# Optimization experiments

Measured on AMD Instinct MI355X. Metric: run time of the kernel, lower is better.

## Reference

```python
import jax, jax.numpy as jnp
import numpy as np

N_NODES = 100000
N_EDGES = 1600000
N_FEAT = 128
HIDDEN = 64
N_CLASSES = 16


def setup_inputs() -> dict:
    key = jax.random.key(0)
    ks = jax.random.split(key, 8)
    x = jax.random.normal(ks[0], (N_NODES, N_FEAT), dtype=jnp.float32)
    edge_index = jax.random.randint(ks[1], (2, N_EDGES), 0, N_NODES, dtype=jnp.int64)
    def glorot(k, shape):
        lim = float(np.sqrt(6.0 / (shape[0] + shape[1])))
        return jax.random.uniform(k, shape, jnp.float32, -lim, lim)
    return {
        "x": x,
        "edge_index": edge_index,
        "W0": glorot(ks[2], (N_FEAT, HIDDEN)), "b0": jnp.zeros((HIDDEN,), jnp.float32),
        "W1": glorot(ks[3], (HIDDEN, HIDDEN)), "b1": jnp.zeros((HIDDEN,), jnp.float32),
        "W2": glorot(ks[4], (HIDDEN, 2)),      "b2": jnp.zeros((2,), jnp.float32),
        "Wc": glorot(ks[5], (2, N_CLASSES)),   "bc": jnp.zeros((N_CLASSES,), jnp.float32),
    }


def _gcn_conv(x, W, b, src, dst, norm, n_nodes):
    # GCNConv: D^{-1/2} (A + I) D^{-1/2} X W + b, edges already include self-loops
    h = x @ W                                  # transform first (small dim)
    msg = h[src] * norm[:, None]               # gather + per-edge scale
    agg = jax.ops.segment_sum(msg, dst, num_segments=n_nodes)  # scatter-add
    return agg + b


def reference(x, edge_index, W0, b0, W1, b1, W2, b2, Wc, bc):
    n = x.shape[0]
    loops = jnp.arange(n, dtype=edge_index.dtype)
    src = jnp.concatenate([edge_index[0], loops])
    dst = jnp.concatenate([edge_index[1], loops])
    # degree on destination (col), including self-loops
    deg = jax.ops.segment_sum(jnp.ones_like(dst, dtype=x.dtype), dst, num_segments=n)
    dis = jnp.where(deg > 0, jax.lax.rsqrt(deg), 0.0)
    norm = dis[src] * dis[dst]

    h = _gcn_conv(x, W0, b0, src, dst, norm, n)              # layer 0, no activation
    h = jnp.tanh(_gcn_conv(h, W1, b1, src, dst, norm, n))    # layer 1
    h = jnp.tanh(_gcn_conv(h, W2, b2, src, dst, norm, n))    # layer 2 -> [N, 2]
    embeddings = h
    out = embeddings @ Wc + bc                               # [N, num_classes]
    return (out, embeddings)
```

## Files before the change

kernel.cpp:

```cpp
#include <hip/hip_runtime.h>


#define NF 128
#define NH 64
#define NPB 256
#define MAXNB 512
#define CAP 6144
#define A1G 1024

__global__ void k_init0(const int* __restrict__ ei, int* __restrict__ fmt,
                        int* __restrict__ ccnt, int nb16) {
    int i = blockIdx.x * 256 + threadIdx.x;
    if (i < nb16) ccnt[i] = 0;
    if (i == 0) {
        int f = 1;
        #pragma unroll
        for (int k = 1; k < 32; k += 2) if (ei[k] != 0) f = 0;
        *fmt = f;
    }
}

__global__ void __launch_bounds__(256) k_coarse(
        const int* __restrict__ ei, const int* __restrict__ fmt,
        int* __restrict__ ccnt, int* __restrict__ blockbase, int E, int NB) {
    __shared__ int h[MAXNB];
    int sh = *fmt;
    for (int i = threadIdx.x; i < NB; i += 256) h[i] = 0;
    __syncthreads();
    for (long long e = (long long)blockIdx.x * 256 + threadIdx.x; e < E;
         e += (long long)A1G * 256) {
        int d = ei[(long long)(E + e) << sh];
        atomicAdd(&h[d >> 8], 1);
    }
    __syncthreads();
    for (int b = threadIdx.x; b < NB; b += 256) {
        int c = h[b];
        int base = (c > 0) ? atomicAdd(&ccnt[b * 16], c) : 0;
        blockbase[(long long)blockIdx.x * NB + b] = base;
    }
}

__global__ void __launch_bounds__(512) k_cscan(
        const int* __restrict__ ccnt, int* __restrict__ cstart, int NB) {
    __shared__ int s[512];
    int t = threadIdx.x;
    int c = (t < NB) ? ccnt[t * 16] : 0;
    s[t] = c;
    __syncthreads();
    for (int off = 1; off < 512; off <<= 1) {
        int v = s[t];
        int u = (t >= off) ? s[t - off] : 0;
        __syncthreads();
        s[t] = v + u;
        __syncthreads();
    }
    if (t < NB) cstart[t] = s[t] - c;
}

__global__ void __launch_bounds__(256) k_cscatter(
        const int* __restrict__ ei, const int* __restrict__ fmt,
        const int* __restrict__ cstart, const int* __restrict__ blockbase,
        int* __restrict__ pairs, int E, int NB) {
    __shared__ int h[MAXNB];
    __shared__ int bb[MAXNB];
    int sh = *fmt;
    for (int i = threadIdx.x; i < NB; i += 256) {
        h[i] = 0;
        bb[i] = cstart[i] + blockbase[(long long)blockIdx.x * NB + i];
    }
    __syncthreads();
    for (long long e = (long long)blockIdx.x * 256 + threadIdx.x; e < E;
         e += (long long)A1G * 256) {
        int s = ei[(long long)e << sh];
        int d = ei[(long long)(E + e) << sh];
        int b = d >> 8;
        int r = atomicAdd(&h[b], 1);
        pairs[bb[b] + r] = s | ((d & 255) << 17);
    }
}

__global__ void __launch_bounds__(256) k_bucket(
        const int* __restrict__ pairs, const int* __restrict__ ccnt,
        const int* __restrict__ cstart, int* __restrict__ esrc,
        int* __restrict__ cnt, int* __restrict__ start, float* __restrict__ dis,
        int N) {
    __shared__ int words[CAP];
    __shared__ unsigned char rk[CAP];
    __shared__ int h[NPB];
    __shared__ int hs[NPB];
    int b = blockIdx.x;
    int cs = cstart[b];
    int ec = ccnt[b * 16];
    if (ec > CAP) ec = CAP;
    int t = threadIdx.x;
    for (int i = t; i < ec; i += 256) words[i] = pairs[cs + i];
    h[t] = 0;
    __syncthreads();
    for (int i = t; i < ec; i += 256) {
        int ld = words[i] >> 17;
        rk[i] = (unsigned char)atomicAdd(&h[ld], 1);
    }
    __syncthreads();
    int c = h[t];
    hs[t] = c;
    __syncthreads();
    for (int off = 1; off < 256; off <<= 1) {
        int v = hs[t];
        int u = (t >= off) ? hs[t - off] : 0;
        __syncthreads();
        hs[t] = v + u;
        __syncthreads();
    }
    int node = b * NPB + t;
    if (node < N) {
        cnt[node] = c;
        start[node] = cs + hs[t] - c;
        dis[node] = rsqrtf(1.0f + (float)c);
    }
    for (int i = t; i < ec; i += 256) {
        int w = words[i];
        int ld = w >> 17;
        esrc[cs + (hs[ld] - h[ld]) + rk[i]] = w & 0x1FFFF;
    }
}

#define KP3 68
__global__ void __launch_bounds__(256) k_gemm128(
        const float* __restrict__ X, const float* __restrict__ W,
        const float* __restrict__ dis, short* __restrict__ T16,
        float* __restrict__ rs, int n) {
    __shared__ float xs[64 * KP3];
    __shared__ float Ws[64 * NH];
    __shared__ int rmax[64];
    if (threadIdx.x < 64) rmax[threadIdx.x] = 0;
    long long rowbase = (long long)blockIdx.x * 64;
    int c0 = (threadIdx.x & 15) * 4;
    int r0 = (threadIdx.x >> 4) * 4;
    float4 a0{0,0,0,0}, a1{0,0,0,0}, a2{0,0,0,0}, a3{0,0,0,0};
    #pragma unroll
    for (int ph = 0; ph < 2; ++ph) {
        if (ph) __syncthreads();
        const float4* Wp4 = (const float4*)(W + (long long)ph * 64 * NH);
        for (int i = threadIdx.x; i < 64 * NH / 4; i += 256)
            ((float4*)Ws)[i] = Wp4[i];
        const float* Xp = X + rowbase * NF + ph * 64;
        for (int i = threadIdx.x; i < 1024; i += 256) {
            int r = i >> 4, kk = (i & 15) << 2;
            float4 v = (rowbase + r < n)
                           ? *(const float4*)(Xp + r * NF + kk)
                           : make_float4(0.f, 0.f, 0.f, 0.f);
            *(float4*)&xs[r * KP3 + kk] = v;
        }
        __syncthreads();
        const float* x0 = &xs[(r0 + 0) * KP3];
        const float* x1 = &xs[(r0 + 1) * KP3];
        const float* x2 = &xs[(r0 + 2) * KP3];
        const float* x3 = &xs[(r0 + 3) * KP3];
        const float* Wp0 = &Ws[c0];
        #pragma unroll 4
        for (int k4 = 0; k4 < 16; ++k4) {
            float4 xv0 = *(const float4*)(x0 + k4 * 4);
            float4 xv1 = *(const float4*)(x1 + k4 * 4);
            float4 xv2 = *(const float4*)(x2 + k4 * 4);
            float4 xv3 = *(const float4*)(x3 + k4 * 4);
            float4 wa = *(const float4*)(Wp0 + (k4 * 4 + 0) * NH);
            float4 wb = *(const float4*)(Wp0 + (k4 * 4 + 1) * NH);
            float4 wc = *(const float4*)(Wp0 + (k4 * 4 + 2) * NH);
            float4 wd = *(const float4*)(Wp0 + (k4 * 4 + 3) * NH);
            a0.x += xv0.x * wa.x; a0.y += xv0.x * wa.y; a0.z += xv0.x * wa.z; a0.w += xv0.x * wa.w;
            a1.x += xv1.x * wa.x; a1.y += xv1.x * wa.y; a1.z += xv1.x * wa.z; a1.w += xv1.x * wa.w;
            a2.x += xv2.x * wa.x; a2.y += xv2.x * wa.y; a2.z += xv2.x * wa.z; a2.w += xv2.x * wa.w;
            a3.x += xv3.x * wa.x; a3.y += xv3.x * wa.y; a3.z += xv3.x * wa.z; a3.w += xv3.x * wa.w;
            a0.x += xv0.y * wb.x; a0.y += xv0.y * wb.y; a0.z += xv0.y * wb.z; a0.w += xv0.y * wb.w;
            a1.x += xv1.y * wb.x; a1.y += xv1.y * wb.y; a1.z += xv1.y * wb.z; a1.w += xv1.y * wb.w;
            a2.x += xv2.y * wb.x; a2.y += xv2.y * wb.y; a2.z += xv2.y * wb.z; a2.w += xv2.y * wb.w;
            a3.x += xv3.y * wb.x; a3.y += xv3.y * wb.y; a3.z += xv3.y * wb.z; a3.w += xv3.y * wb.w;
            a0.x += xv0.z * wc.x; a0.y += xv0.z * wc.y; a0.z += xv0.z * wc.z; a0.w += xv0.z * wc.w;
            a1.x += xv1.z * wc.x; a1.y += xv1.z * wc.y; a1.z += xv1.z * wc.z; a1.w += xv1.z * wc.w;
            a2.x += xv2.z * wc.x; a2.y += xv2.z * wc.y; a2.z += xv2.z * wc.z; a2.w += xv2.z * wc.w;
            a3.x += xv3.z * wc.x; a3.y += xv3.z * wc.y; a3.z += xv3.z * wc.z; a3.w += xv3.z * wc.w;
            a0.x += xv0.w * wd.x; a0.y += xv0.w * wd.y; a0.z += xv0.w * wd.z; a0.w += xv0.w * wd.w;
            a1.x += xv1.w * wd.x; a1.y += xv1.w * wd.y; a1.z += xv1.w * wd.z; a1.w += xv1.w * wd.w;
            a2.x += xv2.w * wd.x; a2.y += xv2.w * wd.y; a2.z += xv2.w * wd.z; a2.w += xv2.w * wd.w;
            a3.x += xv3.w * wd.x; a3.y += xv3.w * wd.y; a3.z += xv3.w * wd.z; a3.w += xv3.w * wd.w;
        }
    }
    int row = (int)rowbase + r0;
    float d0 = (row + 0 < n) ? dis[row + 0] : 0.0f;
    float d1 = (row + 1 < n) ? dis[row + 1] : 0.0f;
    float d2 = (row + 2 < n) ? dis[row + 2] : 0.0f;
    float d3 = (row + 3 < n) ? dis[row + 3] : 0.0f;
    a0.x *= d0; a0.y *= d0; a0.z *= d0; a0.w *= d0;
    a1.x *= d1; a1.y *= d1; a1.z *= d1; a1.w *= d1;
    a2.x *= d2; a2.y *= d2; a2.z *= d2; a2.w *= d2;
    a3.x *= d3; a3.y *= d3; a3.z *= d3; a3.w *= d3;
    float m0 = fmaxf(fmaxf(fabsf(a0.x), fabsf(a0.y)), fmaxf(fabsf(a0.z), fabsf(a0.w)));
    float m1 = fmaxf(fmaxf(fabsf(a1.x), fabsf(a1.y)), fmaxf(fabsf(a1.z), fabsf(a1.w)));
    float m2 = fmaxf(fmaxf(fabsf(a2.x), fabsf(a2.y)), fmaxf(fabsf(a2.z), fabsf(a2.w)));
    float m3 = fmaxf(fmaxf(fabsf(a3.x), fabsf(a3.y)), fmaxf(fabsf(a3.z), fabsf(a3.w)));
    atomicMax(&rmax[r0 + 0], __float_as_int(m0));
    atomicMax(&rmax[r0 + 1], __float_as_int(m1));
    atomicMax(&rmax[r0 + 2], __float_as_int(m2));
    atomicMax(&rmax[r0 + 3], __float_as_int(m3));
    __syncthreads();
    float M0 = __int_as_float(rmax[r0 + 0]);
    float M1 = __int_as_float(rmax[r0 + 1]);
    float M2 = __int_as_float(rmax[r0 + 2]);
    float M3 = __int_as_float(rmax[r0 + 3]);
    float i0 = 32767.0f / fmaxf(M0, 1e-20f);
    float i1 = 32767.0f / fmaxf(M1, 1e-20f);
    float i2 = 32767.0f / fmaxf(M2, 1e-20f);
    float i3 = 32767.0f / fmaxf(M3, 1e-20f);
    const float ks = 1.0f / 32767.0f;
    if (row + 0 < n) {
        short4 q = { (short)__float2int_rn(a0.x * i0), (short)__float2int_rn(a0.y * i0),
                     (short)__float2int_rn(a0.z * i0), (short)__float2int_rn(a0.w * i0) };
        *(short4*)&T16[(long long)(row + 0) * NH + c0] = q;
        if (c0 == 0) rs[row + 0] = M0 * ks;
    }
    if (row + 1 < n) {
        short4 q = { (short)__float2int_rn(a1.x * i1), (short)__float2int_rn(a1.y * i1),
                     (short)__float2int_rn(a1.z * i1), (short)__float2int_rn(a1.w * i1) };
        *(short4*)&T16[(long long)(row + 1) * NH + c0] = q;
        if (c0 == 0) rs[row + 1] = M1 * ks;
    }
    if (row + 2 < n) {
        short4 q = { (short)__float2int_rn(a2.x * i2), (short)__float2int_rn(a2.y * i2),
                     (short)__float2int_rn(a2.z * i2), (short)__float2int_rn(a2.w * i2) };
        *(short4*)&T16[(long long)(row + 2) * NH + c0] = q;
        if (c0 == 0) rs[row + 2] = M2 * ks;
    }
    if (row + 3 < n) {
        short4 q = { (short)__float2int_rn(a3.x * i3), (short)__float2int_rn(a3.y * i3),
                     (short)__float2int_rn(a3.z * i3), (short)__float2int_rn(a3.w * i3) };
        *(short4*)&T16[(long long)(row + 3) * NH + c0] = q;
        if (c0 == 0) rs[row + 3] = M3 * ks;
    }
}

#define EDGE_A(J) {                                                           \
    int s_ = __builtin_amdgcn_readlane(sA, (J));                              \
    float f_ = __int_as_float(__builtin_amdgcn_readlane(fAb, (J)));           \
    accA = fmaf(f_, (float)(T + s_ * NH)[lane], accA); }
#define EDGE_B(J) {                                                           \
    int s_ = __builtin_amdgcn_readlane(sB, (J));                              \
    float f_ = __int_as_float(__builtin_amdgcn_readlane(fBb, (J)));           \
    accB = fmaf(f_, (float)(T + s_ * NH)[lane], accB); }

#define SEG_GATHER2                                                           \
    int lane = threadIdx.x & 63;                                              \
    int na = blockIdx.x * 8 + (threadIdx.x >> 6) * 2;                         \
    int nb_ = na + 1;                                                         \
    if (na >= n) return;                                                      \
    bool hasB = (nb_ < n);                                                    \
    float dia = dis[na];                                                      \
    float dib = hasB ? dis[nb_] : 0.0f;                                       \
    int ga = cnt[na], sta = start[na];                                        \
    int gb = hasB ? cnt[nb_] : 0;                                             \
    int stb = hasB ? start[nb_] : 0;                                          \
    float accA = rs[na] * (float)T[na * NH + lane];                           \
    float accB = hasB ? rs[nb_] * (float)T[nb_ * NH + lane] : 0.0f;           \
    int gmax = ga > gb ? ga : gb;                                             \
    for (int base = 0; base < gmax; base += 64) {                             \
        int ma = ga - base; ma = ma < 0 ? 0 : (ma > 64 ? 64 : ma);            \
        int mb = gb - base; mb = mb < 0 ? 0 : (mb > 64 ? 64 : mb);            \
        int sA = 0, sB = 0; float fA = 0.0f, fB = 0.0f;                       \
        if (lane < ma) { sA = esrc[sta + base + lane]; fA = rs[sA]; }         \
        if (lane < mb) { sB = esrc[stb + base + lane]; fB = rs[sB]; }         \
        int fAb = __float_as_int(fA), fBb = __float_as_int(fB);               \
        int mmin = ma < mb ? ma : mb;                                         \
        int j = 0;                                                            \
        for (; j + 3 < mmin; j += 4) {                                        \
            EDGE_A(j + 0) EDGE_B(j + 0)                                       \
            EDGE_A(j + 1) EDGE_B(j + 1)                                       \
            EDGE_A(j + 2) EDGE_B(j + 2)                                       \
            EDGE_A(j + 3) EDGE_B(j + 3)                                       \
        }                                                                     \
        int jA = j, jB = j;                                                   \
        for (; jA + 3 < ma; jA += 4) {                                        \
            EDGE_A(jA + 0) EDGE_A(jA + 1) EDGE_A(jA + 2) EDGE_A(jA + 3)       \
        }                                                                     \
        for (; jA < ma; ++jA) EDGE_A(jA)                                      \
        for (; jB + 3 < mb; jB += 4) {                                        \
            EDGE_B(jB + 0) EDGE_B(jB + 1) EDGE_B(jB + 2) EDGE_B(jB + 3)       \
        }                                                                     \
        for (; jB < mb; ++jB) EDGE_B(jB)                                      \
    }

__global__ void __launch_bounds__(256) k_seg0t(
        const short* __restrict__ T, const float* __restrict__ rs,
        const int* __restrict__ esrc, const int* __restrict__ start,
        const int* __restrict__ cnt, const float* __restrict__ dis,
        const float* __restrict__ b0, const float* __restrict__ W1,
        short* __restrict__ To, float* __restrict__ rso, int n) {
    __shared__ float W1s[NH * NH];
    for (int i = threadIdx.x; i < NH * NH / 4; i += 256)
        ((float4*)W1s)[i] = ((const float4*)W1)[i];
    __syncthreads();
    SEG_GATHER2
    float bv = b0[lane];
    float hA = dia * accA + bv;
    float hB = dib * accB + bv;
    float oA = 0.0f, oB = 0.0f;
    #pragma unroll
    for (int c = 0; c < 64; ++c) {
        float wv = W1s[c * NH + lane];
        float ha = __int_as_float(__builtin_amdgcn_readlane(__float_as_int(hA), c));
        float hb = __int_as_float(__builtin_amdgcn_readlane(__float_as_int(hB), c));
        oA = fmaf(ha, wv, oA);
        oB = fmaf(hb, wv, oB);
    }
    oA *= dia;
    oB *= dib;
    float mA = fabsf(oA), mB = fabsf(oB);
    #pragma unroll
    for (int msk = 32; msk; msk >>= 1) {
        mA = fmaxf(mA, __shfl_xor(mA, msk, 64));
        mB = fmaxf(mB, __shfl_xor(mB, msk, 64));
    }
    float iA = 32767.0f / fmaxf(mA, 1e-20f);
    float iB = 32767.0f / fmaxf(mB, 1e-20f);
    const float ks = 1.0f / 32767.0f;
    To[(long long)na * NH + lane] = (short)__float2int_rn(oA * iA);
    if (lane == 0) rso[na] = mA * ks;
    if (hasB) {
        To[(long long)nb_ * NH + lane] = (short)__float2int_rn(oB * iB);
        if (lane == 0) rso[nb_] = mB * ks;
    }
}

__global__ void __launch_bounds__(256) k_seg1f(
        const short* __restrict__ T, const float* __restrict__ rs,
        const int* __restrict__ esrc, const int* __restrict__ start,
        const int* __restrict__ cnt, const float* __restrict__ dis,
        const float* __restrict__ b1, const float* __restrict__ W2,
        float2* __restrict__ t2, int n) {
    SEG_GATHER2
    float bv = b1[lane];
    float2 w = ((const float2*)W2)[lane];
    float tA = tanhf(dia * accA + bv);
    float p0 = tA * w.x, p1 = tA * w.y;
    float tB = hasB ? tanhf(dib * accB + bv) : 0.0f;
    float q0 = tB * w.x, q1 = tB * w.y;
    #pragma unroll
    for (int msk = 32; msk; msk >>= 1) {
        p0 += __shfl_xor(p0, msk, 64);
        p1 += __shfl_xor(p1, msk, 64);
        q0 += __shfl_xor(q0, msk, 64);
        q1 += __shfl_xor(q1, msk, 64);
    }
    if (lane == 0) {
        t2[na] = make_float2(dia * p0, dia * p1);
        if (hasB) t2[nb_] = make_float2(dib * q0, dib * q1);
    }
}

__global__ void __launch_bounds__(256) k_seg2f(
        const float2* __restrict__ T2, const int* __restrict__ esrc,
        const int* __restrict__ start, const int* __restrict__ cnt,
        const float* __restrict__ dis, const float* __restrict__ b2,
        const float* __restrict__ Wc, const float* __restrict__ bc,
        float* __restrict__ out, float* __restrict__ emb, int n) {
    __shared__ float Wcs[32];
    __shared__ float bcs[16];
    if (threadIdx.x < 32) Wcs[threadIdx.x] = Wc[threadIdx.x];
    if (threadIdx.x < 16) bcs[threadIdx.x] = bc[threadIdx.x];
    __syncthreads();
    int i = blockIdx.x * 256 + threadIdx.x;
    if (i >= n) return;
    float di = dis[i];
    int g = cnt[i], st = start[i];
    float2 self = T2[i];
    float a0 = self.x, a1 = self.y;
    int j = 0;
    for (; j + 7 < g; j += 8) {
        int e0 = esrc[st+j],   e1 = esrc[st+j+1], e2 = esrc[st+j+2], e3 = esrc[st+j+3];
        int e4 = esrc[st+j+4], e5 = esrc[st+j+5], e6 = esrc[st+j+6], e7 = esrc[st+j+7];
        float2 v0 = T2[e0], v1 = T2[e1], v2 = T2[e2], v3 = T2[e3];
        float2 v4 = T2[e4], v5 = T2[e5], v6 = T2[e6], v7 = T2[e7];
        a0 += v0.x + v1.x + v2.x + v3.x + v4.x + v5.x + v6.x + v7.x;
        a1 += v0.y + v1.y + v2.y + v3.y + v4.y + v5.y + v6.y + v7.y;
    }
    for (; j < g; ++j) {
        float2 v = T2[esrc[st + j]];
        a0 += v.x; a1 += v.y;
    }
    float e0 = tanhf(a0 * di + b2[0]);
    float e1 = tanhf(a1 * di + b2[1]);
    *(float2*)&emb[(long long)i * 2] = make_float2(e0, e1);
    float* op = &out[(long long)i * 16];
    #pragma unroll
    for (int c4 = 0; c4 < 4; ++c4) {
        float4 o;
        o.x = e0 * Wcs[c4*4+0] + e1 * Wcs[16 + c4*4+0] + bcs[c4*4+0];
        o.y = e0 * Wcs[c4*4+1] + e1 * Wcs[16 + c4*4+1] + bcs[c4*4+1];
        o.z = e0 * Wcs[c4*4+2] + e1 * Wcs[16 + c4*4+2] + bcs[c4*4+2];
        o.w = e0 * Wcs[c4*4+3] + e1 * Wcs[16 + c4*4+3] + bcs[c4*4+3];
        *(float4*)&op[c4 * 4] = o;
    }
}

extern "C" void kernel_launch(void* const* d_in, const int* in_sizes, int n_in,
                              void* d_out, int out_size, void* d_ws, size_t ws_size,
                              hipStream_t stream) {
    const float* x  = (const float*)d_in[0];
    const int*   ei = (const int*)  d_in[1];
    const float* W0 = (const float*)d_in[2];
    const float* b0 = (const float*)d_in[3];
    const float* W1 = (const float*)d_in[4];
    const float* b1 = (const float*)d_in[5];
    const float* W2 = (const float*)d_in[6];
    const float* b2 = (const float*)d_in[7];
    const float* Wc = (const float*)d_in[8];
    const float* bc = (const float*)d_in[9];

    int N = in_sizes[0] / NF;
    int E = in_sizes[1] / 2;
    int NB = (N + NPB - 1) / NPB;

    float* out = (float*)d_out;
    float* emb = out + (long long)N * 16;

    short*  T16a = (short*)d_ws;
    char*   r2   = (char*)d_ws + (long long)N * NH * 2;
    short*  T16b = (short*)r2;
    float2* t2   = (float2*)(r2 + (long long)N * NH * 2);
    float*  rs_b = (float*)(r2 + (long long)N * NH * 2 + (long long)N * 8);
    float*  dis  = (float*)((char*)d_ws + (long long)N * NH * 2 + (long long)N * NH * 4);
    float*  rs_a = dis + N;
    int*    cnt   = (int*)(rs_a + N);
    int*    start = cnt + N;
    int*    esrc  = start + N;
    int*    fmt   = esrc + E;

    int* pairs     = (int*)d_ws;
    int* blockbase = pairs + E;
    int* ccnt      = blockbase + (long long)A1G * NB;
    int* cstart    = ccnt + NB * 16;

    int nb_n  = (N + 255) / 256;
    int nb_g  = (N + 63) / 64;
    int nb_s2 = (N + 7) / 8;
    int nb_i0 = (NB * 16 + 255) / 256;

    k_init0   <<<nb_i0, 256, 0, stream>>>(ei, fmt, ccnt, NB * 16);
    k_coarse  <<<A1G, 256, 0, stream>>>(ei, fmt, ccnt, blockbase, E, NB);
    k_cscan   <<<1, 512, 0, stream>>>(ccnt, cstart, NB);
    k_cscatter<<<A1G, 256, 0, stream>>>(ei, fmt, cstart, blockbase, pairs, E, NB);
    k_bucket  <<<NB, 256, 0, stream>>>(pairs, ccnt, cstart, esrc, cnt, start, dis, N);

    k_gemm128 <<<nb_g, 256, 0, stream>>>(x, W0, dis, T16a, rs_a, N);

    k_seg0t   <<<nb_s2, 256, 0, stream>>>(T16a, rs_a, esrc, start, cnt, dis, b0,
                                          W1, T16b, rs_b, N);

    k_seg1f   <<<nb_s2, 256, 0, stream>>>(T16b, rs_b, esrc, start, cnt, dis, b1,
                                          W2, t2, N);

    k_seg2f   <<<nb_n, 256, 0, stream>>>(t2, esrc, start, cnt, dis, b2, Wc, bc,
                                         out, emb, N);
}
```

Before: 333.3 us.

## Store layer-1 features in fp32 and parallelize final-layer gather across 16 lanes

The seg0t kernel now writes its transformed features as plain fp32 instead of per-row int16 quantization with a scale. Dropping the scale removes the per-edge scale lookup and the readlane from the layer-1 gather, in exchange for twice the gather bytes per edge. The final layer now assigns 16 lanes per node with a shuffle reduction instead of one thread per node. This shortens serial per-thread edge loops and balances load across degree variation. The t2 buffer is relocated to alias the start of the workspace, which the T16a buffer already occupies.

```diff
diff --git a/kernel.cpp b/kernel.cpp
--- a/kernel.cpp
+++ b/kernel.cpp
@@ -247,7 +247,14 @@
     float f_ = __int_as_float(__builtin_amdgcn_readlane(fBb, (J)));           \
     accB = fmaf(f_, (float)(T + s_ * NH)[lane], accB); }
 
-#define SEG_GATHER2                                                           \
+#define EDGE_A32(J) {                                                         \
+    int s_ = __builtin_amdgcn_readlane(sA, (J));                              \
+    accA += (Tf + s_ * NH)[lane]; }
+#define EDGE_B32(J) {                                                         \
+    int s_ = __builtin_amdgcn_readlane(sB, (J));                              \
+    accB += (Tf + s_ * NH)[lane]; }
+
+#define SEG_GATHER2_I16                                                       \
     int lane = threadIdx.x & 63;                                              \
     int na = blockIdx.x * 8 + (threadIdx.x >> 6) * 2;                         \
     int nb_ = na + 1;                                                         \
@@ -287,17 +294,56 @@
         for (; jB < mb; ++jB) EDGE_B(jB)                                      \
     }
 
+#define SEG_GATHER2_F32                                                       \
+    int lane = threadIdx.x & 63;                                              \
+    int na = blockIdx.x * 8 + (threadIdx.x >> 6) * 2;                         \
+    int nb_ = na + 1;                                                         \
+    if (na >= n) return;                                                      \
+    bool hasB = (nb_ < n);                                                    \
+    float dia = dis[na];                                                      \
+    float dib = hasB ? dis[nb_] : 0.0f;                                       \
+    int ga = cnt[na], sta = start[na];                                        \
+    int gb = hasB ? cnt[nb_] : 0;                                             \
+    int stb = hasB ? start[nb_] : 0;                                          \
+    float accA = Tf[na * NH + lane];                                          \
+    float accB = hasB ? Tf[nb_ * NH + lane] : 0.0f;                           \
+    int gmax = ga > gb ? ga : gb;                                             \
+    for (int base = 0; base < gmax; base += 64) {                             \
+        int ma = ga - base; ma = ma < 0 ? 0 : (ma > 64 ? 64 : ma);            \
+        int mb = gb - base; mb = mb < 0 ? 0 : (mb > 64 ? 64 : mb);            \
+        int sA = 0, sB = 0;                                                   \
+        if (lane < ma) sA = esrc[sta + base + lane];                          \
+        if (lane < mb) sB = esrc[stb + base + lane];                          \
+        int mmin = ma < mb ? ma : mb;                                         \
+        int j = 0;                                                            \
+        for (; j + 3 < mmin; j += 4) {                                        \
+            EDGE_A32(j + 0) EDGE_B32(j + 0)                                   \
+            EDGE_A32(j + 1) EDGE_B32(j + 1)                                   \
+            EDGE_A32(j + 2) EDGE_B32(j + 2)                                   \
+            EDGE_A32(j + 3) EDGE_B32(j + 3)                                   \
+        }                                                                     \
+        int jA = j, jB = j;                                                   \
+        for (; jA + 3 < ma; jA += 4) {                                        \
+            EDGE_A32(jA + 0) EDGE_A32(jA + 1) EDGE_A32(jA + 2) EDGE_A32(jA + 3) \
+        }                                                                     \
+        for (; jA < ma; ++jA) EDGE_A32(jA)                                    \
+        for (; jB + 3 < mb; jB += 4) {                                        \
+            EDGE_B32(jB + 0) EDGE_B32(jB + 1) EDGE_B32(jB + 2) EDGE_B32(jB + 3) \
+        }                                                                     \
+        for (; jB < mb; ++jB) EDGE_B32(jB)                                    \
+    }
+
 __global__ void __launch_bounds__(256) k_seg0t(
         const short* __restrict__ T, const float* __restrict__ rs,
         const int* __restrict__ esrc, const int* __restrict__ start,
         const int* __restrict__ cnt, const float* __restrict__ dis,
         const float* __restrict__ b0, const float* __restrict__ W1,
-        short* __restrict__ To, float* __restrict__ rso, int n) {
+        float* __restrict__ To, int n) {
     __shared__ float W1s[NH * NH];
     for (int i = threadIdx.x; i < NH * NH / 4; i += 256)
         ((float4*)W1s)[i] = ((const float4*)W1)[i];
     __syncthreads();
-    SEG_GATHER2
+    SEG_GATHER2_I16
     float bv = b0[lane];
     float hA = dia * accA + bv;
     float hB = dib * accB + bv;
@@ -310,32 +356,16 @@
         oA = fmaf(ha, wv, oA);
         oB = fmaf(hb, wv, oB);
     }
-    oA *= dia;
-    oB *= dib;
-    float mA = fabsf(oA), mB = fabsf(oB);
-    #pragma unroll
-    for (int msk = 32; msk; msk >>= 1) {
-        mA = fmaxf(mA, __shfl_xor(mA, msk, 64));
-        mB = fmaxf(mB, __shfl_xor(mB, msk, 64));
-    }
-    float iA = 32767.0f / fmaxf(mA, 1e-20f);
-    float iB = 32767.0f / fmaxf(mB, 1e-20f);
-    const float ks = 1.0f / 32767.0f;
-    To[(long long)na * NH + lane] = (short)__float2int_rn(oA * iA);
-    if (lane == 0) rso[na] = mA * ks;
-    if (hasB) {
-        To[(long long)nb_ * NH + lane] = (short)__float2int_rn(oB * iB);
-        if (lane == 0) rso[nb_] = mB * ks;
-    }
+    To[(long long)na * NH + lane] = oA * dia;
+    if (hasB) To[(long long)nb_ * NH + lane] = oB * dib;
 }
 
 __global__ void __launch_bounds__(256) k_seg1f(
-        const short* __restrict__ T, const float* __restrict__ rs,
-        const int* __restrict__ esrc, const int* __restrict__ start,
-        const int* __restrict__ cnt, const float* __restrict__ dis,
-        const float* __restrict__ b1, const float* __restrict__ W2,
-        float2* __restrict__ t2, int n) {
-    SEG_GATHER2
+        const float* __restrict__ Tf, const int* __restrict__ esrc,
+        const int* __restrict__ start, const int* __restrict__ cnt,
+        const float* __restrict__ dis, const float* __restrict__ b1,
+        const float* __restrict__ W2, float2* __restrict__ t2, int n) {
+    SEG_GATHER2_F32
     float bv = b1[lane];
     float2 w = ((const float2*)W2)[lane];
     float tA = tanhf(dia * accA + bv);
@@ -361,42 +391,38 @@
         const float* __restrict__ dis, const float* __restrict__ b2,
         const float* __restrict__ Wc, const float* __restrict__ bc,
         float* __restrict__ out, float* __restrict__ emb, int n) {
-    __shared__ float Wcs[32];
-    __shared__ float bcs[16];
-    if (threadIdx.x < 32) Wcs[threadIdx.x] = Wc[threadIdx.x];
-    if (threadIdx.x < 16) bcs[threadIdx.x] = bc[threadIdx.x];
-    __syncthreads();
-    int i = blockIdx.x * 256 + threadIdx.x;
+    int lane = threadIdx.x & 63;
+    int sub = lane >> 4;
+    int sl = lane & 15;
+    int i = blockIdx.x * 16 + (threadIdx.x >> 6) * 4 + sub;
     if (i >= n) return;
     float di = dis[i];
     int g = cnt[i], st = start[i];
-    float2 self = T2[i];
-    float a0 = self.x, a1 = self.y;
-    int j = 0;
-    for (; j + 7 < g; j += 8) {
-        int e0 = esrc[st+j],   e1 = esrc[st+j+1], e2 = esrc[st+j+2], e3 = esrc[st+j+3];
-        int e4 = esrc[st+j+4], e5 = esrc[st+j+5], e6 = esrc[st+j+6], e7 = esrc[st+j+7];
-        float2 v0 = T2[e0], v1 = T2[e1], v2 = T2[e2], v3 = T2[e3];
-        float2 v4 = T2[e4], v5 = T2[e5], v6 = T2[e6], v7 = T2[e7];
-        a0 += v0.x + v1.x + v2.x + v3.x + v4.x + v5.x + v6.x + v7.x;
-        a1 += v0.y + v1.y + v2.y + v3.y + v4.y + v5.y + v6.y + v7.y;
-    }
-    for (; j < g; ++j) {
+    float a0 = 0.0f, a1 = 0.0f;
+    for (int j = sl; j < g; j += 16) {
         float2 v = T2[esrc[st + j]];
         a0 += v.x; a1 += v.y;
     }
+    if (sl == 0) {
+        float2 s = T2[i];
+        a0 += s.x; a1 += s.y;
+    }
+    #pragma unroll
+    for (int msk = 8; msk; msk >>= 1) {
+        a0 += __shfl_xor(a0, msk, 64);
+        a1 += __shfl_xor(a1, msk, 64);
+    }
     float e0 = tanhf(a0 * di + b2[0]);
     float e1 = tanhf(a1 * di + b2[1]);
-    *(float2*)&emb[(long long)i * 2] = make_float2(e0, e1);
-    float* op = &out[(long long)i * 16];
-    #pragma unroll
-    for (int c4 = 0; c4 < 4; ++c4) {
+    if (sl == 0) *(float2*)&emb[(long long)i * 2] = make_float2(e0, e1);
+    if (sl < 4) {
+        int c = sl * 4;
         float4 o;
-        o.x = e0 * Wcs[c4*4+0] + e1 * Wcs[16 + c4*4+0] + bcs[c4*4+0];
-        o.y = e0 * Wcs[c4*4+1] + e1 * Wcs[16 + c4*4+1] + bcs[c4*4+1];
-        o.z = e0 * Wcs[c4*4+2] + e1 * Wcs[16 + c4*4+2] + bcs[c4*4+2];
-        o.w = e0 * Wcs[c4*4+3] + e1 * Wcs[16 + c4*4+3] + bcs[c4*4+3];
-        *(float4*)&op[c4 * 4] = o;
+        o.x = e0 * Wc[c + 0] + e1 * Wc[16 + c + 0] + bc[c + 0];
+        o.y = e0 * Wc[c + 1] + e1 * Wc[16 + c + 1] + bc[c + 1];
+        o.z = e0 * Wc[c + 2] + e1 * Wc[16 + c + 2] + bc[c + 2];
+        o.w = e0 * Wc[c + 3] + e1 * Wc[16 + c + 3] + bc[c + 3];
+        *(float4*)&out[(long long)i * 16 + c] = o;
     }
 }
 
@@ -422,25 +448,23 @@
     float* emb = out + (long long)N * 16;
 
     short*  T16a = (short*)d_ws;
-    char*   r2   = (char*)d_ws + (long long)N * NH * 2;
-    short*  T16b = (short*)r2;
-    float2* t2   = (float2*)(r2 + (long long)N * NH * 2);
-    float*  rs_b = (float*)(r2 + (long long)N * NH * 2 + (long long)N * 8);
+    float*  T32b = (float*)((char*)d_ws + (long long)N * NH * 2);
     float*  dis  = (float*)((char*)d_ws + (long long)N * NH * 2 + (long long)N * NH * 4);
     float*  rs_a = dis + N;
     int*    cnt   = (int*)(rs_a + N);
     int*    start = cnt + N;
     int*    esrc  = start + N;
     int*    fmt   = esrc + E;
+    float2* t2    = (float2*)d_ws;
 
     int* pairs     = (int*)d_ws;
     int* blockbase = pairs + E;
     int* ccnt      = blockbase + (long long)A1G * NB;
     int* cstart    = ccnt + NB * 16;
 
-    int nb_n  = (N + 255) / 256;
     int nb_g  = (N + 63) / 64;
     int nb_s2 = (N + 7) / 8;
+    int nb_2f = (N + 15) / 16;
     int nb_i0 = (NB * 16 + 255) / 256;
 
     k_init0   <<<nb_i0, 256, 0, stream>>>(ei, fmt, ccnt, NB * 16);
@@ -452,11 +476,11 @@
     k_gemm128 <<<nb_g, 256, 0, stream>>>(x, W0, dis, T16a, rs_a, N);
 
     k_seg0t   <<<nb_s2, 256, 0, stream>>>(T16a, rs_a, esrc, start, cnt, dis, b0,
-                                          W1, T16b, rs_b, N);
-
-    k_seg1f   <<<nb_s2, 256, 0, stream>>>(T16b, rs_b, esrc, start, cnt, dis, b1,
+                                          W1, T32b, N);
+
+    k_seg1f   <<<nb_s2, 256, 0, stream>>>(T32b, esrc, start, cnt, dis, b1,
                                           W2, t2, N);
 
-    k_seg2f   <<<nb_n, 256, 0, stream>>>(t2, esrc, start, cnt, dis, b2, Wc, bc,
-                                         out, emb, N);
-}
+    k_seg2f   <<<nb_2f, 256, 0, stream>>>(t2, esrc, start, cnt, dis, b2, Wc, bc,
+                                          out, emb, N);
+}
```

Result: slower. 353.1 us (+6.0%).
